# Performance work log

Hardware: AMD Instinct MI355X
Metric: run time of the kernel (lower is better)

Reference implementation:

```python
import jax, jax.numpy as jnp
import numpy as np

B, S, V = 8, 8192, 64
D, DV, DT, H = 256, 32, 256, 8
DH = D // H

def setup_inputs() -> dict:
    key = jax.random.key(0)
    ks = jax.random.split(key, 24)
    def p(i, shape, s=0.02):
        return jax.random.normal(ks[i], shape, jnp.float32) * s
    return {
        'times': jax.random.uniform(ks[0], (B, S), jnp.float32),
        'feature_ids': jax.random.randint(ks[1], (B, S), 0, V),
        'values': jax.random.normal(ks[2], (B, S), jnp.float32),
        'valid_mask': jax.random.randint(ks[3], (B, S), 0, 2).astype(bool),
        'me_w': p(4, (D,), 1.0), 'me_b': p(5, (D,)),
        'var_emb': p(6, (V, DV), 1.0),
        'time_w': p(7, (DT,), 1.0), 'time_b': p(8, (DT,)),
        'agg_w': p(9, (D + DT, D - DV)), 'agg_b': p(10, (D - DV,)),
        'wq': p(11, (D, D)), 'bq': p(12, (D,)),
        'wk': p(13, (D, D)), 'bk': p(14, (D,)),
        'wv': p(15, (D, D)), 'bv': p(16, (D,)),
        'wo': p(17, (D, D)), 'bo': p(18, (D,)),
        'cw1': p(19, (D, D)), 'cb1': p(20, (D,)),
        'cw2': p(21, (D, 1)), 'cb2': p(22, (1,)),
    }

def reference(times, feature_ids, values, valid_mask,
              me_w, me_b, var_emb, time_w, time_b, agg_w, agg_b,
              wq, bq, wk, bk, wv, bv, wo, bo, cw1, cb1, cw2, cb2):
    # Embeddings: measurement [B,S,D], variate [B,S,DV], time [B,S,DT]
    e_l = values[..., None] * me_w + me_b
    v_l = var_emb[feature_ids]
    u_l = times[..., None] * time_w + time_b
    eu = jnp.concatenate([e_l, u_l], axis=-1)                   # [B,S,D+DT]
    h_l = jnp.concatenate([v_l, eu @ agg_w + agg_b], axis=-1)   # [B,S,D]

    # Vectorized masked segment mean per variate (replaces Python loop)
    var_mask = (feature_ids[:, None, :] == jnp.arange(V)[None, :, None]) \
               & valid_mask[:, None, :]                         # [B,V,S] bool
    mf = var_mask.astype(h_l.dtype)
    sums = jnp.einsum('bvs,bsd->bvd', mf, h_l)
    counts = jnp.clip(mf.sum(-1), 1.0)                          # [B,V]
    f_mean = sums / counts[..., None]                           # [B,V,D]

    # Grouped cross-attention: one query per variate, shared K/V = h_l
    kpm = ~var_mask                                             # key padding mask
    all_masked = ~var_mask.any(-1)                              # [B,V]
    kpm = kpm.at[:, :, 0].set(kpm[:, :, 0] & ~all_masked)       # unmask pos 0 if empty

    q = (f_mean @ wq + bq).reshape(B, V, H, DH)
    k = (h_l @ wk + bk).reshape(B, S, H, DH)
    v = (h_l @ wv + bv).reshape(B, S, H, DH)
    scores = jnp.einsum('bvhd,bshd->bvhs', q, k) / np.sqrt(DH)  # [B,V,H,S]
    neg = jnp.finfo(scores.dtype).min
    scores = jnp.where(kpm[:, :, None, :], neg, scores)
    attn = jax.nn.softmax(scores, axis=-1)
    ctx = jnp.einsum('bvhs,bshd->bvhd', attn, v).reshape(B, V, D)
    f_var = ctx @ wo + bo                                       # [B,V,D]

    f = f_var.mean(axis=1)                                      # [B,D]
    out = jax.nn.relu(f @ cw1 + cb1) @ cw2 + cb2                # [B,1]
    return out
```

## Files before the change

### kernel.cpp

```cpp
#include <hip/hip_runtime.h>
#include <hip/hip_bf16.h>
#include <math.h>

#define BB 8
#define SS 8192
#define VV 64
#define AGG_OUT 224

#define WS_FLAGS 0
#define WS_A     16
#define WS_C     240
#define WS_D     464
#define WS_AQ    688
#define WS_CQ    944
#define WS_DQ    1200
#define WS_AK    1456
#define WS_CK    1712
#define WS_DK    1968
#define WS_AV    2224
#define WS_CV    2480
#define WS_DV    2736
#define WS_WQE   2992
#define WS_WKE   19376
#define WS_WVE   35760
#define WS_CSUM  52144
#define WS_BINS  54192
#define WS_COEF  66480
#define WS_SP    82864

__device__ __forceinline__ float ldf(const void* p, int idx, int fm) {
  if (fm) {
    unsigned int u = ((const unsigned short*)p)[idx];
    return __uint_as_float(u << 16);
  }
  return ((const float*)p)[idx];
}

__device__ __forceinline__ bool mask_at(const void* p, int idx, int mm) {
  switch (mm) {
    case 0: return ((const int*)p)[idx] != 0;
    case 1: return ((const float*)p)[idx] != 0.0f;
    case 2: return ((const unsigned short*)p)[idx] != 0;
    default: return ((const unsigned char*)p)[idx] != 0;
  }
}

__device__ __forceinline__ unsigned int fkey(float f) {
  unsigned int u = __float_as_uint(f);
  return (u & 0x80000000u) ? ~u : (u | 0x80000000u);
}
__device__ __forceinline__ float funkey(unsigned int k) {
  unsigned int u = (k & 0x80000000u) ? (k ^ 0x80000000u) : ~k;
  return __uint_as_float(u);
}

__device__ __forceinline__ int detect_fm_block(const void* times) {
  __shared__ int cntR;
  int tid = threadIdx.x;
  if (tid == 0) cntR = 0;
  __syncthreads();
  const unsigned int* tw = (const unsigned int*)times;
  int local = 0;
  for (int i = tid; i < 1024; i += 256) {
    unsigned int lo = tw[i] & 0xFFFFu;
    if (lo >= 0x3800u && lo < 0x3F80u) local++;
  }
  atomicAdd(&cntR, local);
  __syncthreads();
  int r = (cntR > 512) ? 1 : 0;
  __syncthreads();
  return r;
}

__device__ __forceinline__ int detect_mm_block(const void* mask) {
  __shared__ int f01, ff32, fbf;
  int tid = threadIdx.x;
  if (tid == 0) { f01 = 1; ff32 = 1; fbf = 1; }
  __syncthreads();
  const unsigned int* mw = (const unsigned int*)mask;
  int l01 = 1, lf32 = 1, lbf = 1;
  for (int i = tid; i < 2048; i += 256) {
    unsigned int w = mw[i];
    if (w > 1u) l01 = 0;
    if (!(w == 0u || w == 0x3F800000u)) lf32 = 0;
    unsigned int h0 = w & 0xFFFFu, h1 = w >> 16;
    if (!((h0 == 0u || h0 == 0x3F80u) && (h1 == 0u || h1 == 0x3F80u))) lbf = 0;
  }
  if (!l01) atomicAnd(&f01, 0);
  if (!lf32) atomicAnd(&ff32, 0);
  if (!lbf) atomicAnd(&fbf, 0);
  __syncthreads();
  int r = f01 ? 0 : (ff32 ? 1 : (fbf ? 2 : 3));
  __syncthreads();
  return r;
}

__global__ void __launch_bounds__(256) k_front(const void* times, const void* values,
                                               const int* fids, const void* mask,
                                               const void* me_w, const void* me_b,
                                               const void* time_w, const void* time_b,
                                               const void* agg_w, const void* agg_b,
                                               float* ws) {
  int blk = blockIdx.x, tid = threadIdx.x;
  if (blk < 224) {
    int fm = detect_fm_block(times);
    int j = blk, i = tid;
    float w0 = ldf(agg_w, i * AGG_OUT + j, fm);
    float w1 = ldf(agg_w, (256 + i) * AGG_OUT + j, fm);
    float sa = ldf(me_w, i, fm) * w0;
    float sc = ldf(time_w, i, fm) * w1;
    float sd = ldf(me_b, i, fm) * w0 + ldf(time_b, i, fm) * w1;
    #pragma unroll
    for (int off = 32; off >= 1; off >>= 1) {
      sa += __shfl_xor(sa, off);
      sc += __shfl_xor(sc, off);
      sd += __shfl_xor(sd, off);
    }
    __shared__ float r[3][4];
    int wid = i >> 6;
    if ((i & 63) == 0) { r[0][wid] = sa; r[1][wid] = sc; r[2][wid] = sd; }
    __syncthreads();
    if (i == 0) {
      ws[WS_A + j] = r[0][0] + r[0][1] + r[0][2] + r[0][3];
      ws[WS_C + j] = r[1][0] + r[1][1] + r[1][2] + r[1][3];
      ws[WS_D + j] = r[2][0] + r[2][1] + r[2][2] + r[2][3] + ldf(agg_b, j, fm);
    }
  } else if (blk < 288) {
    int fm = detect_fm_block(times);
    int mm = detect_mm_block(mask);
    int sblk = blk - 224, b = sblk >> 3, chunk = sblk & 7;
    __shared__ float hc[64], hsv[64], hst[64];
    __shared__ unsigned int hvn[64], hvx[64], htn[64], htx[64];
    if (tid < 64) {
      hc[tid] = 0.f; hsv[tid] = 0.f; hst[tid] = 0.f;
      hvn[tid] = 0xFFFFFFFFu; hvx[tid] = 0u;
      htn[tid] = 0xFFFFFFFFu; htx[tid] = 0u;
    }
    __syncthreads();
    #pragma unroll
    for (int k = 0; k < 4; k++) {
      int idx = b * SS + chunk * 1024 + k * 256 + tid;
      if (mask_at(mask, idx, mm)) {
        int f = fids[idx];
        float val = ldf(values, idx, fm), tim = ldf(times, idx, fm);
        atomicAdd(&hc[f], 1.0f);
        atomicAdd(&hsv[f], val);
        atomicAdd(&hst[f], tim);
        unsigned int vk = fkey(val), tk = fkey(tim);
        atomicMin(&hvn[f], vk); atomicMax(&hvx[f], vk);
        atomicMin(&htn[f], tk); atomicMax(&htx[f], tk);
      }
    }
    __syncthreads();
    if (tid < 64) {
      int base = WS_SP + (sblk * 64 + tid) * 8;
      ws[base + 0] = hc[tid];
      ws[base + 1] = hsv[tid];
      ws[base + 2] = hst[tid];
      ((unsigned int*)ws)[base + 3] = hvn[tid];
      ((unsigned int*)ws)[base + 4] = hvx[tid];
      ((unsigned int*)ws)[base + 5] = htn[tid];
      ((unsigned int*)ws)[base + 6] = htx[tid];
    }
  } else {
    int zblk = blk - 288;
    for (int i = zblk * 256 + tid; i < 14336; i += 2048) ws[WS_CSUM + i] = 0.f;
    if (zblk == 0) {
      int fm = detect_fm_block(times);
      int mm = detect_mm_block(mask);
      if (tid == 0) { ((int*)ws)[0] = fm; ((int*)ws)[1] = mm; }
    }
  }
}

__global__ void __launch_bounds__(256) k_pre(const void* wq, const void* wk,
                                             const void* wv, const void* bk,
                                             const void* bv, const void* var_emb,
                                             float* ws) {
  int fm = ((const int*)ws)[0];
  int blk = blockIdx.x, tid = threadIdx.x;
  if (blk < 24) {
    int X = blk >> 3, dg = blk & 7;
    const void* w = (X == 0) ? wq : (X == 1) ? wk : wv;
    __shared__ float sha[224], shc[224], shd[224];
    if (tid < 224) {
      sha[tid] = ws[WS_A + tid];
      shc[tid] = ws[WS_C + tid];
      shd[tid] = ws[WS_D + tid];
    }
    __syncthreads();
    int dsub = tid & 31, jg = tid >> 5;
    int d = dg * 32 + dsub;
    float sa = 0.f, sc = 0.f, sd = 0.f;
    #pragma unroll 4
    for (int jj = 0; jj < 28; jj++) {
      int j = jg * 28 + jj;
      float ww = ldf(w, (32 + j) * 256 + d, fm);
      sa += sha[j] * ww; sc += shc[j] * ww; sd += shd[j] * ww;
    }
    __shared__ float ps[3][8][32];
    ps[0][jg][dsub] = sa; ps[1][jg][dsub] = sc; ps[2][jg][dsub] = sd;
    __syncthreads();
    if (tid < 32) {
      float ra = 0.f, rc = 0.f, rd = 0.f;
      #pragma unroll
      for (int g = 0; g < 8; g++) {
        ra += ps[0][g][tid]; rc += ps[1][g][tid]; rd += ps[2][g][tid];
      }
      int dd = dg * 32 + tid;
      if (X == 1) rd += ldf(bk, dd, fm);
      if (X == 2) rd += ldf(bv, dd, fm);
      int base = (X == 0) ? WS_AQ : (X == 1) ? WS_AK : WS_AV;
      ws[base + dd] = ra;
      ws[base + 256 + dd] = rc;
      ws[base + 512 + dd] = rd;
    }
  } else {
    int idx = blk - 24, X = idx >> 6, v = idx & 63, d = tid;
    const void* w = (X == 0) ? wq : (X == 1) ? wk : wv;
    float s = 0.f;
    #pragma unroll 8
    for (int i = 0; i < 32; i++)
      s += ldf(var_emb, v * 32 + i, fm) * ldf(w, i * 256 + d, fm);
    int base = (X == 0) ? WS_WQE : (X == 1) ? WS_WKE : WS_WVE;
    ws[base + v * 256 + d] = s;
  }
}

__global__ void __launch_bounds__(256) k_coef(const void* values, const void* times,
                                              const int* fids, const void* bq,
                                              float* ws) {
  int fm = ((const int*)ws)[0];
  int bv = blockIdx.x, b = bv >> 6, v = bv & 63;
  int tid = threadIdx.x, h = tid >> 5;
  __shared__ float sp[8][8];
  if (tid < 64) {
    int sl = tid >> 3, c = tid & 7;
    sp[sl][c] = ws[WS_SP + ((b * 8 + sl) * 64 + v) * 8 + c];
  }
  __syncthreads();
  float cT = 0.f, svT = 0.f, stT = 0.f;
  unsigned int vnk = 0xFFFFFFFFu, vxk = 0u, tnk = 0xFFFFFFFFu, txk = 0u;
  #pragma unroll
  for (int sl = 0; sl < 8; sl++) {
    cT += sp[sl][0]; svT += sp[sl][1]; stT += sp[sl][2];
    unsigned int a3 = __float_as_uint(sp[sl][3]);
    unsigned int a4 = __float_as_uint(sp[sl][4]);
    unsigned int a5 = __float_as_uint(sp[sl][5]);
    unsigned int a6 = __float_as_uint(sp[sl][6]);
    vnk = min(vnk, a3); vxk = max(vxk, a4);
    tnk = min(tnk, a5); txk = max(txk, a6);
  }
  if (cT == 0.f) {
    int f0 = fids[b * SS];
    float v0 = ldf(values, b * SS, fm), t0 = ldf(times, b * SS, fm);
    float ctx = ws[WS_WVE + f0 * 256 + tid] + ws[WS_DV + tid]
              + v0 * ws[WS_AV + tid] + t0 * ws[WS_CV + tid];
    atomicAdd(&ws[WS_CSUM + b * 256 + tid], ctx);
    return;
  }
  float inv = 1.0f / cT, mv = svT * inv, mt = stT * inv;
  float qv = ldf(bq, tid, fm) + ws[WS_WQE + v * 256 + tid]
           + mv * ws[WS_AQ + tid] + mt * ws[WS_CQ + tid] + ws[WS_DQ + tid];
  qv *= 0.17677669529663687f * 1.4426950408889634f;
  float pA = qv * (ws[WS_WKE + v * 256 + tid] + ws[WS_DK + tid]);
  float pB = qv * ws[WS_AK + tid];
  float pC = qv * ws[WS_CK + tid];
  #pragma unroll
  for (int off = 16; off >= 1; off >>= 1) {
    pA += __shfl_xor(pA, off);
    pB += __shfl_xor(pB, off);
    pC += __shfl_xor(pC, off);
  }
  if ((tid & 31) == 0) {
    float vmn = funkey(vnk), vmx = funkey(vxk);
    float tmn = funkey(tnk), tmx = funkey(txk);
    float m = pA + fmaxf(pB * vmn, pB * vmx) + fmaxf(pC * tmn, pC * tmx);
    int base = WS_COEF + (bv * 8 + h) * 4;
    ws[base + 0] = pA; ws[base + 1] = pB; ws[base + 2] = pC; ws[base + 3] = m;
  }
}

__global__ void __launch_bounds__(256) k_accum(const void* values, const void* times,
                                               const int* fids, const void* mask,
                                               float* ws) {
  int fm = ((const int*)ws)[0], mm = ((const int*)ws)[1];
  int blk = blockIdx.x, tid = threadIdx.x;
  int b = blk >> 4, chunk = blk & 15;
  __shared__ float co[64 * 36];
  __shared__ float bins[64 * 25];
  for (int i = tid; i < 2048; i += 256) {
    int v = i >> 5, r = i & 31;
    co[v * 36 + r] = ws[WS_COEF + b * 2048 + i];
  }
  for (int i = tid; i < 1600; i += 256) bins[i] = 0.f;
  __syncthreads();
  #pragma unroll
  for (int k = 0; k < 2; k++) {
    int idx = b * SS + chunk * 512 + k * 256 + tid;
    if (mask_at(mask, idx, mm)) {
      int f = fids[idx];
      float val = ldf(values, idx, fm), tim = ldf(times, idx, fm);
      #pragma unroll
      for (int h = 0; h < 8; h++) {
        int cb = f * 36 + h * 4;
        float w = exp2f(co[cb] + val * co[cb + 1] + tim * co[cb + 2] - co[cb + 3]);
        int bb = f * 25 + h * 3;
        atomicAdd(&bins[bb], w);
        atomicAdd(&bins[bb + 1], w * val);
        atomicAdd(&bins[bb + 2], w * tim);
      }
    }
  }
  __syncthreads();
  for (int i = tid; i < 1536; i += 256) {
    int f = i / 24, r = i - f * 24;
    float x = bins[f * 25 + r];
    if (x != 0.f) atomicAdd(&ws[WS_BINS + b * 1536 + i], x);
  }
}

__global__ void __launch_bounds__(1024) k_fin(const void* wo, const void* bo,
                                              const void* cw1, const void* cb1,
                                              const void* cw2, const void* cb2,
                                              float* ws, void* out) {
  int fm = ((const int*)ws)[0];
  int b = blockIdx.x, tid = threadIdx.x;
  __shared__ float aa[64][9], tt[64][9], ne[64];
  __shared__ float ps[4][256], cs[256], fv[256], pr[16];
  if (tid < 512) {
    int v = tid >> 3, h = tid & 7;
    int base = WS_BINS + b * 1536 + v * 24 + h * 3;
    float W = ws[base], WV = ws[base + 1], WT = ws[base + 2];
    float iW = (W > 0.f) ? 1.0f / W : 0.f;
    aa[v][h] = WV * iW; tt[v][h] = WT * iW;
    if (h == 0) ne[v] = (W > 0.f) ? 1.f : 0.f;
  }
  __syncthreads();
  int d = tid & 255, vg = tid >> 8, h = d >> 5;
  float accP = 0.f, accA = 0.f, accT = 0.f, accN = 0.f;
  #pragma unroll 4
  for (int k = 0; k < 16; k++) {
    int v = vg * 16 + k;
    float nef = ne[v];
    accP += nef * ws[WS_WVE + v * 256 + d];
    accA += aa[v][h];
    accT += tt[v][h];
    accN += nef;
  }
  ps[vg][d] = accP + accN * ws[WS_DV + d] + accA * ws[WS_AV + d] + accT * ws[WS_CV + d];
  __syncthreads();
  if (tid < 256)
    cs[tid] = (ws[WS_CSUM + b * 256 + tid] + ps[0][tid] + ps[1][tid]
             + ps[2][tid] + ps[3][tid]) * (1.0f / 64.0f);
  __syncthreads();
  float s = 0.f;
  #pragma unroll 8
  for (int k = 0; k < 64; k++) {
    int i = vg * 64 + k;
    s += cs[i] * ldf(wo, i * 256 + d, fm);
  }
  ps[vg][d] = s;
  __syncthreads();
  if (tid < 256) fv[tid] = ps[0][tid] + ps[1][tid] + ps[2][tid] + ps[3][tid]
                         + ldf(bo, tid, fm);
  __syncthreads();
  float t2 = 0.f;
  #pragma unroll 8
  for (int k = 0; k < 64; k++) {
    int i = vg * 64 + k;
    t2 += fv[i] * ldf(cw1, i * 256 + d, fm);
  }
  ps[vg][d] = t2;
  __syncthreads();
  float p = 0.f;
  if (tid < 256) {
    float t = ps[0][tid] + ps[1][tid] + ps[2][tid] + ps[3][tid] + ldf(cb1, tid, fm);
    t = fmaxf(t, 0.f);
    p = t * ldf(cw2, tid, fm);
  }
  #pragma unroll
  for (int off = 32; off >= 1; off >>= 1) p += __shfl_xor(p, off);
  if ((tid & 63) == 0) pr[tid >> 6] = p;
  __syncthreads();
  if (tid == 0) {
    float o = ldf(cb2, 0, fm);
    #pragma unroll
    for (int wgi = 0; wgi < 16; wgi++) o += pr[wgi];
    if (fm) {
      unsigned int x = __float_as_uint(o);
      unsigned int r = (x + 0x7FFFu + ((x >> 16) & 1u)) >> 16;
      ((unsigned short*)out)[b] = (unsigned short)r;
    } else {
      ((float*)out)[b] = o;
    }
  }
}

extern "C" void kernel_launch(void* const* d_in, const int* in_sizes, int n_in,
                              void* d_out, int out_size, void* d_ws, size_t ws_size,
                              hipStream_t stream) {
  const void* times   = d_in[0];
  const int*  fids    = (const int*)d_in[1];
  const void* values  = d_in[2];
  const void* vmask   = d_in[3];
  const void* me_w    = d_in[4];
  const void* me_b    = d_in[5];
  const void* var_emb = d_in[6];
  const void* time_w  = d_in[7];
  const void* time_b  = d_in[8];
  const void* agg_w   = d_in[9];
  const void* agg_b   = d_in[10];
  const void* wq = d_in[11]; const void* bq = d_in[12];
  const void* wk = d_in[13]; const void* bk = d_in[14];
  const void* wv = d_in[15]; const void* bv = d_in[16];
  const void* wo = d_in[17]; const void* bo = d_in[18];
  const void* cw1 = d_in[19]; const void* cb1 = d_in[20];
  const void* cw2 = d_in[21]; const void* cb2 = d_in[22];
  float* ws = (float*)d_ws;

  k_front<<<296, 256, 0, stream>>>(times, values, fids, vmask,
                                   me_w, me_b, time_w, time_b, agg_w, agg_b, ws);
  k_pre<<<216, 256, 0, stream>>>(wq, wk, wv, bk, bv, var_emb, ws);
  k_coef<<<512, 256, 0, stream>>>(values, times, fids, bq, ws);
  k_accum<<<128, 256, 0, stream>>>(values, times, fids, vmask, ws);
  k_fin<<<8, 1024, 0, stream>>>(wo, bo, cw1, cb1, cw2, cb2, ws, d_out);
}
```

Baseline: 149.2 us.

## Fold variate-embedding projections into front kernel and split tail across blocks

The 192 blocks that project the variate embeddings through wq/wk/wv move from k_pre into k_front, since they do not depend on front results. This shortens k_pre to 24 blocks and lets that work overlap with the front pass. The final head kernel is split from 8 per-batch blocks into 16 column-slice blocks that cover all batches. A spin-wait grid barrier on a workspace counter joins them between the wo and cw1 stages, and an atomic accumulator plus a last-block flag produces the output. The barrier depends on all 16 blocks being resident at once, and the atomic float sums add scheduling-dependent ordering to the reduction.

```diff
diff --git a/kernel.cpp b/kernel.cpp
--- a/kernel.cpp
+++ b/kernel.cpp
@@ -27,6 +27,9 @@
 #define WS_BINS  54192
 #define WS_COEF  66480
 #define WS_SP    82864
+#define WS_F     115648
+#define WS_ACC   117696
+#define WS_CNT   117704
 
 __device__ __forceinline__ float ldf(const void* p, int idx, int fm) {
   if (fm) {
@@ -100,6 +103,8 @@
                                                const void* me_w, const void* me_b,
                                                const void* time_w, const void* time_b,
                                                const void* agg_w, const void* agg_b,
+                                               const void* wq, const void* wk,
+                                               const void* wv, const void* var_emb,
                                                float* ws) {
   int blk = blockIdx.x, tid = threadIdx.x;
   if (blk < 224) {
@@ -162,61 +167,18 @@
       ((unsigned int*)ws)[base + 5] = htn[tid];
       ((unsigned int*)ws)[base + 6] = htx[tid];
     }
-  } else {
+  } else if (blk < 296) {
     int zblk = blk - 288;
     for (int i = zblk * 256 + tid; i < 14336; i += 2048) ws[WS_CSUM + i] = 0.f;
+    if (zblk == 1 && tid < 10) ws[WS_ACC + tid] = 0.f;
     if (zblk == 0) {
       int fm = detect_fm_block(times);
       int mm = detect_mm_block(mask);
       if (tid == 0) { ((int*)ws)[0] = fm; ((int*)ws)[1] = mm; }
     }
-  }
-}
-
-__global__ void __launch_bounds__(256) k_pre(const void* wq, const void* wk,
-                                             const void* wv, const void* bk,
-                                             const void* bv, const void* var_emb,
-                                             float* ws) {
-  int fm = ((const int*)ws)[0];
-  int blk = blockIdx.x, tid = threadIdx.x;
-  if (blk < 24) {
-    int X = blk >> 3, dg = blk & 7;
-    const void* w = (X == 0) ? wq : (X == 1) ? wk : wv;
-    __shared__ float sha[224], shc[224], shd[224];
-    if (tid < 224) {
-      sha[tid] = ws[WS_A + tid];
-      shc[tid] = ws[WS_C + tid];
-      shd[tid] = ws[WS_D + tid];
-    }
-    __syncthreads();
-    int dsub = tid & 31, jg = tid >> 5;
-    int d = dg * 32 + dsub;
-    float sa = 0.f, sc = 0.f, sd = 0.f;
-    #pragma unroll 4
-    for (int jj = 0; jj < 28; jj++) {
-      int j = jg * 28 + jj;
-      float ww = ldf(w, (32 + j) * 256 + d, fm);
-      sa += sha[j] * ww; sc += shc[j] * ww; sd += shd[j] * ww;
-    }
-    __shared__ float ps[3][8][32];
-    ps[0][jg][dsub] = sa; ps[1][jg][dsub] = sc; ps[2][jg][dsub] = sd;
-    __syncthreads();
-    if (tid < 32) {
-      float ra = 0.f, rc = 0.f, rd = 0.f;
-      #pragma unroll
-      for (int g = 0; g < 8; g++) {
-        ra += ps[0][g][tid]; rc += ps[1][g][tid]; rd += ps[2][g][tid];
-      }
-      int dd = dg * 32 + tid;
-      if (X == 1) rd += ldf(bk, dd, fm);
-      if (X == 2) rd += ldf(bv, dd, fm);
-      int base = (X == 0) ? WS_AQ : (X == 1) ? WS_AK : WS_AV;
-      ws[base + dd] = ra;
-      ws[base + 256 + dd] = rc;
-      ws[base + 512 + dd] = rd;
-    }
   } else {
-    int idx = blk - 24, X = idx >> 6, v = idx & 63, d = tid;
+    int fm = detect_fm_block(times);
+    int idx = blk - 296, X = idx >> 6, v = idx & 63, d = tid;
     const void* w = (X == 0) ? wq : (X == 1) ? wk : wv;
     float s = 0.f;
     #pragma unroll 8
@@ -224,6 +186,48 @@
       s += ldf(var_emb, v * 32 + i, fm) * ldf(w, i * 256 + d, fm);
     int base = (X == 0) ? WS_WQE : (X == 1) ? WS_WKE : WS_WVE;
     ws[base + v * 256 + d] = s;
+  }
+}
+
+__global__ void __launch_bounds__(256) k_pre(const void* wq, const void* wk,
+                                             const void* wv, const void* bk,
+                                             const void* bv, float* ws) {
+  int fm = ((const int*)ws)[0];
+  int blk = blockIdx.x, tid = threadIdx.x;
+  int X = blk >> 3, dg = blk & 7;
+  const void* w = (X == 0) ? wq : (X == 1) ? wk : wv;
+  __shared__ float sha[224], shc[224], shd[224];
+  if (tid < 224) {
+    sha[tid] = ws[WS_A + tid];
+    shc[tid] = ws[WS_C + tid];
+    shd[tid] = ws[WS_D + tid];
+  }
+  __syncthreads();
+  int dsub = tid & 31, jg = tid >> 5;
+  int d = dg * 32 + dsub;
+  float sa = 0.f, sc = 0.f, sd = 0.f;
+  #pragma unroll 4
+  for (int jj = 0; jj < 28; jj++) {
+    int j = jg * 28 + jj;
+    float ww = ldf(w, (32 + j) * 256 + d, fm);
+    sa += sha[j] * ww; sc += shc[j] * ww; sd += shd[j] * ww;
+  }
+  __shared__ float ps[3][8][32];
+  ps[0][jg][dsub] = sa; ps[1][jg][dsub] = sc; ps[2][jg][dsub] = sd;
+  __syncthreads();
+  if (tid < 32) {
+    float ra = 0.f, rc = 0.f, rd = 0.f;
+    #pragma unroll
+    for (int g = 0; g < 8; g++) {
+      ra += ps[0][g][tid]; rc += ps[1][g][tid]; rd += ps[2][g][tid];
+    }
+    int dd = dg * 32 + tid;
+    if (X == 1) rd += ldf(bk, dd, fm);
+    if (X == 2) rd += ldf(bv, dd, fm);
+    int base = (X == 0) ? WS_AQ : (X == 1) ? WS_AK : WS_AV;
+    ws[base + dd] = ra;
+    ws[base + 256 + dd] = rc;
+    ws[base + 512 + dd] = rd;
   }
 }
 
@@ -320,79 +324,124 @@
   }
 }
 
-__global__ void __launch_bounds__(1024) k_fin(const void* wo, const void* bo,
-                                              const void* cw1, const void* cb1,
-                                              const void* cw2, const void* cb2,
-                                              float* ws, void* out) {
+__global__ void __launch_bounds__(1024) k_tail(const void* wo, const void* bo,
+                                               const void* cw1, const void* cb1,
+                                               const void* cw2, const void* cb2,
+                                               float* ws, void* out) {
   int fm = ((const int*)ws)[0];
-  int b = blockIdx.x, tid = threadIdx.x;
-  __shared__ float aa[64][9], tt[64][9], ne[64];
-  __shared__ float ps[4][256], cs[256], fv[256], pr[16];
-  if (tid < 512) {
-    int v = tid >> 3, h = tid & 7;
+  int blk = blockIdx.x, tid = threadIdx.x;
+  int c0 = blk * 16;
+  unsigned int* cnt = (unsigned int*)ws + WS_CNT;
+  __shared__ float aaL[8][64][8];
+  __shared__ float ttL[8][64][8];
+  __shared__ float neL[8][64];
+  __shared__ float csL[8][256];
+  __shared__ float wSl[256][16];
+  __shared__ float part[8][8][16];
+  __shared__ int lastB;
+
+  for (int idx = tid; idx < 4096; idx += 1024) {
+    int b = idx >> 9, v = (idx >> 3) & 63, h = idx & 7;
     int base = WS_BINS + b * 1536 + v * 24 + h * 3;
-    float W = ws[base], WV = ws[base + 1], WT = ws[base + 2];
+    float W = ws[base], Wv = ws[base + 1], Wt = ws[base + 2];
     float iW = (W > 0.f) ? 1.0f / W : 0.f;
-    aa[v][h] = WV * iW; tt[v][h] = WT * iW;
-    if (h == 0) ne[v] = (W > 0.f) ? 1.f : 0.f;
-  }
-  __syncthreads();
-  int d = tid & 255, vg = tid >> 8, h = d >> 5;
-  float accP = 0.f, accA = 0.f, accT = 0.f, accN = 0.f;
-  #pragma unroll 4
-  for (int k = 0; k < 16; k++) {
-    int v = vg * 16 + k;
-    float nef = ne[v];
-    accP += nef * ws[WS_WVE + v * 256 + d];
-    accA += aa[v][h];
-    accT += tt[v][h];
-    accN += nef;
-  }
-  ps[vg][d] = accP + accN * ws[WS_DV + d] + accA * ws[WS_AV + d] + accT * ws[WS_CV + d];
-  __syncthreads();
-  if (tid < 256)
-    cs[tid] = (ws[WS_CSUM + b * 256 + tid] + ps[0][tid] + ps[1][tid]
-             + ps[2][tid] + ps[3][tid]) * (1.0f / 64.0f);
-  __syncthreads();
-  float s = 0.f;
-  #pragma unroll 8
-  for (int k = 0; k < 64; k++) {
-    int i = vg * 64 + k;
-    s += cs[i] * ldf(wo, i * 256 + d, fm);
-  }
-  ps[vg][d] = s;
-  __syncthreads();
-  if (tid < 256) fv[tid] = ps[0][tid] + ps[1][tid] + ps[2][tid] + ps[3][tid]
-                         + ldf(bo, tid, fm);
-  __syncthreads();
-  float t2 = 0.f;
-  #pragma unroll 8
-  for (int k = 0; k < 64; k++) {
-    int i = vg * 64 + k;
-    t2 += fv[i] * ldf(cw1, i * 256 + d, fm);
-  }
-  ps[vg][d] = t2;
-  __syncthreads();
-  float p = 0.f;
-  if (tid < 256) {
-    float t = ps[0][tid] + ps[1][tid] + ps[2][tid] + ps[3][tid] + ldf(cb1, tid, fm);
-    t = fmaxf(t, 0.f);
-    p = t * ldf(cw2, tid, fm);
-  }
-  #pragma unroll
-  for (int off = 32; off >= 1; off >>= 1) p += __shfl_xor(p, off);
-  if ((tid & 63) == 0) pr[tid >> 6] = p;
+    aaL[b][v][h] = Wv * iW;
+    ttL[b][v][h] = Wt * iW;
+    if (h == 0) neL[b][v] = (W > 0.f) ? 1.f : 0.f;
+  }
+  {
+    int i = tid >> 2, c = (tid & 3) * 4;
+    #pragma unroll
+    for (int u = 0; u < 4; u++)
+      wSl[i][c + u] = ldf(wo, i * 256 + c0 + c + u, fm);
+  }
+  __syncthreads();
+  for (int o = tid; o < 2048; o += 1024) {
+    int b = o >> 8, d = o & 255, h = d >> 5;
+    float accP = 0.f, accA = 0.f, accT = 0.f, accN = 0.f;
+    #pragma unroll 4
+    for (int v = 0; v < VV; v++) {
+      float nef = neL[b][v];
+      accP += nef * ws[WS_WVE + v * 256 + d];
+      accA += aaL[b][v][h];
+      accT += ttL[b][v][h];
+      accN += nef;
+    }
+    csL[b][d] = (ws[WS_CSUM + b * 256 + d] + accP + accN * ws[WS_DV + d]
+               + accA * ws[WS_AV + d] + accT * ws[WS_CV + d]) * (1.0f / 64.0f);
+  }
+  __syncthreads();
+  {
+    int ig = tid >> 7, r = tid & 127, b = r >> 4, c = r & 15;
+    float s = 0.f;
+    #pragma unroll 8
+    for (int k = 0; k < 32; k++) {
+      int i = ig * 32 + k;
+      s += csL[b][i] * wSl[i][c];
+    }
+    part[ig][b][c] = s;
+  }
+  __syncthreads();
+  if (tid < 128) {
+    int b = tid >> 4, c = tid & 15;
+    float s = 0.f;
+    #pragma unroll
+    for (int g = 0; g < 8; g++) s += part[g][b][c];
+    ws[WS_F + blk * 128 + b * 16 + c] = s + ldf(bo, c0 + c, fm);
+  }
+  __threadfence();
   __syncthreads();
   if (tid == 0) {
-    float o = ldf(cb2, 0, fm);
-    #pragma unroll
-    for (int wgi = 0; wgi < 16; wgi++) o += pr[wgi];
+    atomicAdd(&cnt[0], 1u);
+    while (atomicAdd(&cnt[0], 0u) < 16u) {}
+  }
+  __syncthreads();
+  __threadfence();
+  for (int idx = tid; idx < 2048; idx += 1024) {
+    int b = idx >> 8, d = idx & 255;
+    csL[b][d] = ws[WS_F + (d >> 4) * 128 + b * 16 + (d & 15)];
+  }
+  {
+    int i = tid >> 2, c = (tid & 3) * 4;
+    #pragma unroll
+    for (int u = 0; u < 4; u++)
+      wSl[i][c + u] = ldf(cw1, i * 256 + c0 + c + u, fm);
+  }
+  __syncthreads();
+  {
+    int ig = tid >> 7, r = tid & 127, b = r >> 4, c = r & 15;
+    float s = 0.f;
+    #pragma unroll 8
+    for (int k = 0; k < 32; k++) {
+      int i = ig * 32 + k;
+      s += csL[b][i] * wSl[i][c];
+    }
+    part[ig][b][c] = s;
+  }
+  __syncthreads();
+  if (tid < 128) {
+    int b = tid >> 4, c = tid & 15;
+    float s = 0.f;
+    #pragma unroll
+    for (int g = 0; g < 8; g++) s += part[g][b][c];
+    float t = fmaxf(s + ldf(cb1, c0 + c, fm), 0.f);
+    float pp = t * ldf(cw2, c0 + c, fm);
+    #pragma unroll
+    for (int off = 1; off < 16; off <<= 1) pp += __shfl_xor(pp, off);
+    if (c == 0) atomicAdd(&ws[WS_ACC + b], pp);
+  }
+  __threadfence();
+  __syncthreads();
+  if (tid == 0) lastB = (atomicAdd(&cnt[1], 1u) == 15u) ? 1 : 0;
+  __syncthreads();
+  if (lastB && tid < 8) {
+    float o = atomicAdd(&ws[WS_ACC + tid], 0.0f) + ldf(cb2, 0, fm);
     if (fm) {
       unsigned int x = __float_as_uint(o);
       unsigned int r = (x + 0x7FFFu + ((x >> 16) & 1u)) >> 16;
-      ((unsigned short*)out)[b] = (unsigned short)r;
+      ((unsigned short*)out)[tid] = (unsigned short)r;
     } else {
-      ((float*)out)[b] = o;
+      ((float*)out)[tid] = o;
     }
   }
 }
@@ -419,10 +468,11 @@
   const void* cw2 = d_in[21]; const void* cb2 = d_in[22];
   float* ws = (float*)d_ws;
 
-  k_front<<<296, 256, 0, stream>>>(times, values, fids, vmask,
-                                   me_w, me_b, time_w, time_b, agg_w, agg_b, ws);
-  k_pre<<<216, 256, 0, stream>>>(wq, wk, wv, bk, bv, var_emb, ws);
+  k_front<<<488, 256, 0, stream>>>(times, values, fids, vmask,
+                                   me_w, me_b, time_w, time_b, agg_w, agg_b,
+                                   wq, wk, wv, var_emb, ws);
+  k_pre<<<24, 256, 0, stream>>>(wq, wk, wv, bk, bv, ws);
   k_coef<<<512, 256, 0, stream>>>(values, times, fids, bq, ws);
   k_accum<<<128, 256, 0, stream>>>(values, times, fids, vmask, ws);
-  k_fin<<<8, 1024, 0, stream>>>(wo, bo, cw1, cb1, cw2, cb2, ws, d_out);
-}
+  k_tail<<<16, 1024, 0, stream>>>(wo, bo, cw1, cb1, cw2, cb2, ws, d_out);
+}
```

New measurement: 162.9 us. 9.1% more time.

## Merge coefficient and accumulation kernels using per-batch ticket counters

Applied to the files above, without the earlier changes.

Combines k_coef and k_accum into a single 640-block launch. The first 512 blocks compute the attention coefficients and increment a per-batch ticket, and the remaining 128 blocks spin until their batch's ticket reaches 64 before accumulating. The aim is to remove one kernel launch and the full grid barrier between the two stages. The accumulator blocks depend on the producer blocks being scheduled, which risks deadlock or spinning if the grid does not fit at once. The spin loop and atomic loads also add their own overhead.

```diff
diff --git a/kernel.cpp b/kernel.cpp
--- a/kernel.cpp
+++ b/kernel.cpp
@@ -27,6 +27,8 @@
 #define WS_BINS  54192
 #define WS_COEF  66480
 #define WS_SP    82864
+#define WS_ACC   117696
+#define WS_CNT   117704
 
 __device__ __forceinline__ float ldf(const void* p, int idx, int fm) {
   if (fm) {
@@ -165,6 +167,7 @@
   } else {
     int zblk = blk - 288;
     for (int i = zblk * 256 + tid; i < 14336; i += 2048) ws[WS_CSUM + i] = 0.f;
+    if (zblk == 1 && tid < 16) ws[WS_ACC + tid] = 0.f;
     if (zblk == 0) {
       int fm = detect_fm_block(times);
       int mm = detect_mm_block(mask);
@@ -227,96 +230,106 @@
   }
 }
 
-__global__ void __launch_bounds__(256) k_coef(const void* values, const void* times,
-                                              const int* fids, const void* bq,
-                                              float* ws) {
+__global__ void __launch_bounds__(256) k_cacc(const void* values, const void* times,
+                                              const int* fids, const void* mask,
+                                              const void* bq, float* ws) {
   int fm = ((const int*)ws)[0];
-  int bv = blockIdx.x, b = bv >> 6, v = bv & 63;
-  int tid = threadIdx.x, h = tid >> 5;
-  __shared__ float sp[8][8];
-  if (tid < 64) {
-    int sl = tid >> 3, c = tid & 7;
-    sp[sl][c] = ws[WS_SP + ((b * 8 + sl) * 64 + v) * 8 + c];
-  }
-  __syncthreads();
-  float cT = 0.f, svT = 0.f, stT = 0.f;
-  unsigned int vnk = 0xFFFFFFFFu, vxk = 0u, tnk = 0xFFFFFFFFu, txk = 0u;
-  #pragma unroll
-  for (int sl = 0; sl < 8; sl++) {
-    cT += sp[sl][0]; svT += sp[sl][1]; stT += sp[sl][2];
-    unsigned int a3 = __float_as_uint(sp[sl][3]);
-    unsigned int a4 = __float_as_uint(sp[sl][4]);
-    unsigned int a5 = __float_as_uint(sp[sl][5]);
-    unsigned int a6 = __float_as_uint(sp[sl][6]);
-    vnk = min(vnk, a3); vxk = max(vxk, a4);
-    tnk = min(tnk, a5); txk = max(txk, a6);
-  }
-  if (cT == 0.f) {
-    int f0 = fids[b * SS];
-    float v0 = ldf(values, b * SS, fm), t0 = ldf(times, b * SS, fm);
-    float ctx = ws[WS_WVE + f0 * 256 + tid] + ws[WS_DV + tid]
-              + v0 * ws[WS_AV + tid] + t0 * ws[WS_CV + tid];
-    atomicAdd(&ws[WS_CSUM + b * 256 + tid], ctx);
-    return;
-  }
-  float inv = 1.0f / cT, mv = svT * inv, mt = stT * inv;
-  float qv = ldf(bq, tid, fm) + ws[WS_WQE + v * 256 + tid]
-           + mv * ws[WS_AQ + tid] + mt * ws[WS_CQ + tid] + ws[WS_DQ + tid];
-  qv *= 0.17677669529663687f * 1.4426950408889634f;
-  float pA = qv * (ws[WS_WKE + v * 256 + tid] + ws[WS_DK + tid]);
-  float pB = qv * ws[WS_AK + tid];
-  float pC = qv * ws[WS_CK + tid];
-  #pragma unroll
-  for (int off = 16; off >= 1; off >>= 1) {
-    pA += __shfl_xor(pA, off);
-    pB += __shfl_xor(pB, off);
-    pC += __shfl_xor(pC, off);
-  }
-  if ((tid & 31) == 0) {
-    float vmn = funkey(vnk), vmx = funkey(vxk);
-    float tmn = funkey(tnk), tmx = funkey(txk);
-    float m = pA + fmaxf(pB * vmn, pB * vmx) + fmaxf(pC * tmn, pC * tmx);
-    int base = WS_COEF + (bv * 8 + h) * 4;
-    ws[base + 0] = pA; ws[base + 1] = pB; ws[base + 2] = pC; ws[base + 3] = m;
-  }
-}
-
-__global__ void __launch_bounds__(256) k_accum(const void* values, const void* times,
-                                               const int* fids, const void* mask,
-                                               float* ws) {
-  int fm = ((const int*)ws)[0], mm = ((const int*)ws)[1];
   int blk = blockIdx.x, tid = threadIdx.x;
-  int b = blk >> 4, chunk = blk & 15;
-  __shared__ float co[64 * 36];
-  __shared__ float bins[64 * 25];
-  for (int i = tid; i < 2048; i += 256) {
-    int v = i >> 5, r = i & 31;
-    co[v * 36 + r] = ws[WS_COEF + b * 2048 + i];
-  }
-  for (int i = tid; i < 1600; i += 256) bins[i] = 0.f;
-  __syncthreads();
-  #pragma unroll
-  for (int k = 0; k < 2; k++) {
-    int idx = b * SS + chunk * 512 + k * 256 + tid;
-    if (mask_at(mask, idx, mm)) {
-      int f = fids[idx];
-      float val = ldf(values, idx, fm), tim = ldf(times, idx, fm);
+  unsigned int* ticket = (unsigned int*)(ws + WS_CNT);
+  if (blk < 512) {
+    int bv = blk, b = bv >> 6, v = bv & 63;
+    int h = tid >> 5;
+    __shared__ float sp[8][8];
+    if (tid < 64) {
+      int sl = tid >> 3, c = tid & 7;
+      sp[sl][c] = ws[WS_SP + ((b * 8 + sl) * 64 + v) * 8 + c];
+    }
+    __syncthreads();
+    float cT = 0.f, svT = 0.f, stT = 0.f;
+    unsigned int vnk = 0xFFFFFFFFu, vxk = 0u, tnk = 0xFFFFFFFFu, txk = 0u;
+    #pragma unroll
+    for (int sl = 0; sl < 8; sl++) {
+      cT += sp[sl][0]; svT += sp[sl][1]; stT += sp[sl][2];
+      unsigned int a3 = __float_as_uint(sp[sl][3]);
+      unsigned int a4 = __float_as_uint(sp[sl][4]);
+      unsigned int a5 = __float_as_uint(sp[sl][5]);
+      unsigned int a6 = __float_as_uint(sp[sl][6]);
+      vnk = min(vnk, a3); vxk = max(vxk, a4);
+      tnk = min(tnk, a5); txk = max(txk, a6);
+    }
+    if (cT == 0.f) {
+      int f0 = fids[b * SS];
+      float v0 = ldf(values, b * SS, fm), t0 = ldf(times, b * SS, fm);
+      float ctx = ws[WS_WVE + f0 * 256 + tid] + ws[WS_DV + tid]
+                + v0 * ws[WS_AV + tid] + t0 * ws[WS_CV + tid];
+      atomicAdd(&ws[WS_CSUM + b * 256 + tid], ctx);
+    } else {
+      float inv = 1.0f / cT, mv = svT * inv, mt = stT * inv;
+      float qv = ldf(bq, tid, fm) + ws[WS_WQE + v * 256 + tid]
+               + mv * ws[WS_AQ + tid] + mt * ws[WS_CQ + tid] + ws[WS_DQ + tid];
+      qv *= 0.17677669529663687f * 1.4426950408889634f;
+      float pA = qv * (ws[WS_WKE + v * 256 + tid] + ws[WS_DK + tid]);
+      float pB = qv * ws[WS_AK + tid];
+      float pC = qv * ws[WS_CK + tid];
       #pragma unroll
-      for (int h = 0; h < 8; h++) {
-        int cb = f * 36 + h * 4;
-        float w = exp2f(co[cb] + val * co[cb + 1] + tim * co[cb + 2] - co[cb + 3]);
-        int bb = f * 25 + h * 3;
-        atomicAdd(&bins[bb], w);
-        atomicAdd(&bins[bb + 1], w * val);
-        atomicAdd(&bins[bb + 2], w * tim);
+      for (int off = 16; off >= 1; off >>= 1) {
+        pA += __shfl_xor(pA, off);
+        pB += __shfl_xor(pB, off);
+        pC += __shfl_xor(pC, off);
       }
-    }
-  }
-  __syncthreads();
-  for (int i = tid; i < 1536; i += 256) {
-    int f = i / 24, r = i - f * 24;
-    float x = bins[f * 25 + r];
-    if (x != 0.f) atomicAdd(&ws[WS_BINS + b * 1536 + i], x);
+      if ((tid & 31) == 0) {
+        float vmn = funkey(vnk), vmx = funkey(vxk);
+        float tmn = funkey(tnk), tmx = funkey(txk);
+        float m = pA + fmaxf(pB * vmn, pB * vmx) + fmaxf(pC * tmn, pC * tmx);
+        int base = WS_COEF + (bv * 8 + h) * 4;
+        atomicExch(&ws[base + 0], pA);
+        atomicExch(&ws[base + 1], pB);
+        atomicExch(&ws[base + 2], pC);
+        atomicExch(&ws[base + 3], m);
+      }
+    }
+    __builtin_amdgcn_s_waitcnt(0);
+    __syncthreads();
+    if (tid == 0) atomicAdd(&ticket[b], 1u);
+  } else {
+    int mm = ((const int*)ws)[1];
+    int ab = blk - 512;
+    int b = ab >> 4, chunk = ab & 15;
+    __shared__ float co[64 * 36];
+    __shared__ float bins[64 * 25];
+    for (int i = tid; i < 1600; i += 256) bins[i] = 0.f;
+    if (tid == 0) {
+      while (atomicAdd(&ticket[b], 0u) < 64u) { __builtin_amdgcn_s_sleep(8); }
+    }
+    __syncthreads();
+    for (int i = tid; i < 2048; i += 256) {
+      int v = i >> 5, r = i & 31;
+      co[v * 36 + r] = atomicAdd(&ws[WS_COEF + b * 2048 + i], 0.0f);
+    }
+    __syncthreads();
+    #pragma unroll
+    for (int k = 0; k < 2; k++) {
+      int idx = b * SS + chunk * 512 + k * 256 + tid;
+      if (mask_at(mask, idx, mm)) {
+        int f = fids[idx];
+        float val = ldf(values, idx, fm), tim = ldf(times, idx, fm);
+        #pragma unroll
+        for (int h = 0; h < 8; h++) {
+          int cb = f * 36 + h * 4;
+          float w = exp2f(co[cb] + val * co[cb + 1] + tim * co[cb + 2] - co[cb + 3]);
+          int bb = f * 25 + h * 3;
+          atomicAdd(&bins[bb], w);
+          atomicAdd(&bins[bb + 1], w * val);
+          atomicAdd(&bins[bb + 2], w * tim);
+        }
+      }
+    }
+    __syncthreads();
+    for (int i = tid; i < 1536; i += 256) {
+      int f = i / 24, r = i - f * 24;
+      float x = bins[f * 25 + r];
+      if (x != 0.f) atomicAdd(&ws[WS_BINS + b * 1536 + i], x);
+    }
   }
 }
 
@@ -422,7 +435,6 @@
   k_front<<<296, 256, 0, stream>>>(times, values, fids, vmask,
                                    me_w, me_b, time_w, time_b, agg_w, agg_b, ws);
   k_pre<<<216, 256, 0, stream>>>(wq, wk, wv, bk, bv, var_emb, ws);
-  k_coef<<<512, 256, 0, stream>>>(values, times, fids, bq, ws);
-  k_accum<<<128, 256, 0, stream>>>(values, times, fids, vmask, ws);
+  k_cacc<<<640, 256, 0, stream>>>(values, times, fids, vmask, bq, ws);
   k_fin<<<8, 1024, 0, stream>>>(wo, bo, cw1, cb1, cw2, cb2, ws, d_out);
 }
```

After: 156.9 us. 1.05x slower.
